# Kernel optimization log

Measured on AMD Instinct MI355X. Metric: run time of the kernel, lower is better.

Reference implementation:

```python
import jax, jax.numpy as jnp
import numpy as np

B, S, E, H, FFN, NQ = 4, 2048, 1024, 16, 4096, 8
DK = E // H
EPS = 1e-5


def setup_inputs() -> dict:
    key = jax.random.key(0)
    ks = jax.random.split(key, 8)
    x = jax.random.normal(ks[0], (B, S, E), dtype=jnp.float32)
    theta = jax.random.normal(ks[1], (NQ,), dtype=jnp.float32)  # RY angles
    w1 = jax.random.normal(ks[2], (FFN, NQ), dtype=jnp.float32) / np.sqrt(NQ)
    b1 = jnp.zeros((FFN,), dtype=jnp.float32)
    w2 = jax.random.normal(ks[3], (E, FFN), dtype=jnp.float32) / np.sqrt(FFN)
    b2 = jnp.zeros((E,), dtype=jnp.float32)
    gamma1 = jnp.ones((E,), dtype=jnp.float32)
    beta1 = jnp.zeros((E,), dtype=jnp.float32)
    gamma2 = jnp.ones((E,), dtype=jnp.float32)
    beta2 = jnp.zeros((E,), dtype=jnp.float32)
    return {"x": x, "theta": theta, "w1": w1, "b1": b1, "w2": w2, "b2": b2,
            "gamma1": gamma1, "beta1": beta1, "gamma2": gamma2, "beta2": beta2}


def _layernorm(h, g, b):
    mu = jnp.mean(h, axis=-1, keepdims=True)
    var = jnp.mean(jnp.square(h - mu), axis=-1, keepdims=True)
    return (h - mu) * jax.lax.rsqrt(var + EPS) * g + b


def _attention(x):
    # q = k = v = separate_heads(x); no projection weights in the original.
    q = x.reshape(B, S, H, DK).transpose(0, 2, 1, 3)  # [B,H,S,DK]
    scores = jnp.einsum("bhqd,bhkd->bhqk", q, q) / np.sqrt(DK)
    probs = jax.nn.softmax(scores, axis=-1)
    out = jnp.einsum("bhqk,bhkd->bhqd", probs, q)
    return out.transpose(0, 2, 1, 3).reshape(B, S, E)


def _ffn_quantum(h, theta, w1, b1, w2, b2):
    # Per-token circuit: RX(x_i) then RY(theta_i) on independent qubits,
    # measure PauliZ -> <Z_i> = cos(x_i) * cos(theta_i). Batched over all tokens.
    qout = jnp.cos(h[..., :NQ]) * jnp.cos(theta)  # [B,S,NQ]
    hid = jax.nn.relu(jnp.einsum("bsq,fq->bsf", qout, w1) + b1)
    return jnp.einsum("bsf,ef->bse", hid, w2) + b2


def reference(x, theta, w1, b1, w2, b2, gamma1, beta1, gamma2, beta2):
    attn_out = _attention(x)
    h = _layernorm(x + attn_out, gamma1, beta1)
    ffn_out = _ffn_quantum(h, theta, w1, b1, w2, b2)
    return _layernorm(h + ffn_out, gamma2, beta2)
```

## Files before the change

kernel.cpp:

```cpp
#include <hip/hip_runtime.h>


#define Bq 4
#define Sq 2048
#define Eq 1024
#define Hq 16
#define DKq 64
#define FFNq 4096
#define NQq 8
#define LOG2E 1.44269504f

typedef unsigned int u32;
typedef unsigned short u16;
typedef _Float16 f16;
typedef f16 f16x8 __attribute__((ext_vector_type(8)));
typedef __fp16 fp16x2 __attribute__((ext_vector_type(2)));
typedef float f32x4 __attribute__((ext_vector_type(4)));

#if __has_builtin(__builtin_amdgcn_exp2f)
#define EXP2F __builtin_amdgcn_exp2f
#else
#define EXP2F exp2f
#endif

#define MFMA(a, b, c) __builtin_amdgcn_mfma_f32_16x16x32_f16((a), (b), (c), 0, 0, 0)

#define GLL(g, l)                                                          \
  __builtin_amdgcn_global_load_lds(                                        \
      (const __attribute__((address_space(1))) u32*)(g),                   \
      (__attribute__((address_space(3))) u32*)(l), 16, 0, 0)

__device__ __forceinline__ u16 f2h(float x) {
  f16 t = (f16)x;
  return __builtin_bit_cast(u16, t);
}
__device__ __forceinline__ float h2f(u16 w) {
  return (float)__builtin_bit_cast(f16, w);
}
#if __has_builtin(__builtin_amdgcn_cvt_pkrtz)
__device__ __forceinline__ u32 pkrtz(float a, float b) {
  fp16x2 r = __builtin_amdgcn_cvt_pkrtz(a, b);
  return __builtin_bit_cast(u32, r);
}
#else
__device__ __forceinline__ u32 pkrtz(float a, float b) {
  return (u32)f2h(a) | ((u32)f2h(b) << 16);
}
#endif

union F8 { f16x8 v; u32 w[4]; u16 h[8]; f16 e[8]; };

__global__ void k_cvt(const float* __restrict__ src, uint4* __restrict__ dst, int n8) {
  int i = blockIdx.x * 256 + threadIdx.x;
  if (i >= n8) return;
  const float4* s = (const float4*)src + 2 * (long)i;
  float4 a = s[0], b = s[1];
  uint4 r;
  r.x = pkrtz(a.x, a.y);
  r.y = pkrtz(a.z, a.w);
  r.z = pkrtz(b.x, b.y);
  r.w = pkrtz(b.z, b.w);
  dst[i] = r;
}

__global__ void k_prep(const float* __restrict__ x, u16* __restrict__ xh,
                       u16* __restrict__ xt) {
  __shared__ u16 tile[64 * 72];
  const int tid = threadIdx.x;
  const int bx = blockIdx.x;
  const int sb = bx & 31, bh = bx >> 5;
  const int b = bh >> 4, h = bh & 15;
  const int s0 = sb * 64;
  const int r = tid >> 2, cq = tid & 3;
  const float* xp = x + ((long)(b * Sq + s0 + r)) * Eq + h * 64 + cq * 16;
  float4 f0 = ((const float4*)xp)[0], f1 = ((const float4*)xp)[1];
  float4 f2 = ((const float4*)xp)[2], f3 = ((const float4*)xp)[3];
  u32 w[8];
  w[0] = pkrtz(f0.x, f0.y); w[1] = pkrtz(f0.z, f0.w);
  w[2] = pkrtz(f1.x, f1.y); w[3] = pkrtz(f1.z, f1.w);
  w[4] = pkrtz(f2.x, f2.y); w[5] = pkrtz(f2.z, f2.w);
  w[6] = pkrtz(f3.x, f3.y); w[7] = pkrtz(f3.z, f3.w);
  uint4* xo = (uint4*)(xh + ((long)(b * Sq + s0 + r)) * Eq + h * 64 + cq * 16);
  xo[0] = make_uint4(w[0], w[1], w[2], w[3]);
  xo[1] = make_uint4(w[4], w[5], w[6], w[7]);
  uint4* tp = (uint4*)(tile + r * 72 + cq * 16);
  tp[0] = make_uint4(w[0], w[1], w[2], w[3]);
  tp[1] = make_uint4(w[4], w[5], w[6], w[7]);
  __syncthreads();
  const int d = tid >> 2, rq = tid & 3;
  u32 o[8];
#pragma unroll
  for (int i = 0; i < 8; ++i) {
    u32 lo = tile[(rq * 16 + 2 * i) * 72 + d];
    u32 hi = tile[(rq * 16 + 2 * i + 1) * 72 + d];
    o[i] = lo | (hi << 16);
  }
  uint4* to = (uint4*)(xt + ((long)(bh * 64 + d)) * Sq + s0 + rq * 16);
  to[0] = make_uint4(o[0], o[1], o[2], o[3]);
  to[1] = make_uint4(o[4], o[5], o[6], o[7]);
}

__global__ __launch_bounds__(512, 4) void k_attn(const u16* __restrict__ xh,
                                                 const u16* __restrict__ xt,
                                                 u16* __restrict__ attn) {
  __shared__ __align__(16) u16 lds[32768];
  u16* Pl = lds + 16384;

  const int tid = threadIdx.x;
  const int wave = tid >> 6, lane = tid & 63;
  const int n = lane & 15, quad = lane >> 4;

  const int bx = blockIdx.x;
  const int qb = bx >> 6, bh = bx & 63;
  const int b = bh >> 4, h = bh & 15;

  const u16* xh_bh = xh + (long)b * Sq * Eq + h * 64;
  const u16* xt_bh = xt + (long)bh * 64 * Sq;

  const float SC = 0.125f * LOG2E;
  F8 qf[2][2];
  float shift[2], lrow[2] = {0.f, 0.f};
#pragma unroll
  for (int nt = 0; nt < 2; ++nt) {
    const int q = qb * 256 + wave * 32 + nt * 16 + n;
    const u16* qp = xh_bh + (long)q * Eq + quad * 8;
    F8 a, c;
    a.v = *(const f16x8*)qp;
    c.v = *(const f16x8*)(qp + 32);
    float s2 = 0.f;
#pragma unroll
    for (int i = 0; i < 8; ++i) {
      float va = (float)a.e[i], vc = (float)c.e[i];
      s2 += va * va + vc * vc;
      qf[nt][0].e[i] = a.e[i] * (f16)SC;
      qf[nt][1].e[i] = c.e[i] * (f16)SC;
    }
    s2 += __shfl_xor(s2, 16);
    s2 += __shfl_xor(s2, 32);
    shift[nt] = SC * s2;
  }

  const int r8 = lane >> 3;
  const int cl = (lane & 7) ^ r8;
  const u16* gK = xh_bh + (long)(wave * 8 + r8) * Eq + cl * 8;
  const u16* gV = xt_bh + (long)(wave * 8 + r8) * Sq + cl * 8;
  const int lK = wave * 512;
  const int lV = 4096 + wave * 512;

  u16* cur = lds;
  u16* nxt = lds + 8192;

  GLL(gK, cur + lK);
  GLL(gV, cur + lV);
  gK += 64 * Eq;
  gV += 64;

  f32x4 O[2][4] = {};
  u16* Pw = Pl + wave * 2048;

  for (int kb = 0; kb < Sq / 64; ++kb) {
    __syncthreads();
    if (kb < Sq / 64 - 1) {
      GLL(gK, nxt + lK);
      GLL(gV, nxt + lV);
      gK += 64 * Eq;
      gV += 64;
    }
    u16* Kl = cur;
    u16* Vt = cur + 4096;

    f32x4 ST[2][4];
#pragma unroll
    for (int nt = 0; nt < 2; ++nt) {
      const float ms = -shift[nt];
#pragma unroll
      for (int mt = 0; mt < 4; ++mt) {
        ST[nt][mt][0] = ms; ST[nt][mt][1] = ms;
        ST[nt][mt][2] = ms; ST[nt][mt][3] = ms;
      }
    }
    __builtin_amdgcn_s_setprio(1);
#pragma unroll
    for (int mt = 0; mt < 4; ++mt) {
#pragma unroll
      for (int c = 0; c < 2; ++c) {
        f16x8 af = *(const f16x8*)(Kl + (mt * 16 + n) * 64 +
                                   (((c * 4 + quad) ^ (n & 7)) * 8));
#pragma unroll
        for (int nt = 0; nt < 2; ++nt)
          ST[nt][mt] = MFMA(af, qf[nt][c].v, ST[nt][mt]);
      }
    }
    __builtin_amdgcn_s_setprio(0);

#pragma unroll
    for (int nt = 0; nt < 2; ++nt) {
      float ls = 0.f;
#pragma unroll
      for (int mt = 0; mt < 4; ++mt) {
        float p0 = EXP2F(ST[nt][mt][0]);
        float p1 = EXP2F(ST[nt][mt][1]);
        float p2 = EXP2F(ST[nt][mt][2]);
        float p3 = EXP2F(ST[nt][mt][3]);
        ls += (p0 + p1) + (p2 + p3);
        const int ch = 2 * mt + (quad >> 1);
        *(uint2*)(Pw + nt * 1024 + n * 64 + ((ch ^ (n & 7)) * 8) + (quad & 1) * 4) =
            make_uint2(pkrtz(p0, p1), pkrtz(p2, p3));
      }
      lrow[nt] += ls;
    }

    __builtin_amdgcn_s_setprio(1);
#pragma unroll
    for (int c = 0; c < 2; ++c) {
      const int pc = ((c * 4 + quad) ^ (n & 7)) * 8;
      f16x8 pf[2];
#pragma unroll
      for (int nt = 0; nt < 2; ++nt)
        pf[nt] = *(const f16x8*)(Pw + nt * 1024 + n * 64 + pc);
#pragma unroll
      for (int dt = 0; dt < 4; ++dt) {
        f16x8 vf = *(const f16x8*)(Vt + (dt * 16 + n) * 64 + pc);
#pragma unroll
        for (int nt = 0; nt < 2; ++nt) O[nt][dt] = MFMA(vf, pf[nt], O[nt][dt]);
      }
    }
    __builtin_amdgcn_s_setprio(0);
    u16* t = cur; cur = nxt; nxt = t;
  }

#pragma unroll
  for (int nt = 0; nt < 2; ++nt) {
    float l = lrow[nt];
    l += __shfl_xor(l, 16);
    l += __shfl_xor(l, 32);
    const float inv = 1.0f / l;
    const int q = qb * 256 + wave * 32 + nt * 16 + n;
    u16* op = attn + (long)b * Sq * Eq + (long)q * Eq + h * 64;
#pragma unroll
    for (int dt = 0; dt < 4; ++dt) {
      u32 w0 = pkrtz(O[nt][dt][0] * inv, O[nt][dt][1] * inv);
      u32 w1 = pkrtz(O[nt][dt][2] * inv, O[nt][dt][3] * inv);
      *(uint2*)(op + dt * 16 + quad * 4) = make_uint2(w0, w1);
    }
  }
}

__global__ void k_ln1(const u16* __restrict__ xh, const u16* __restrict__ attn,
                      const float* __restrict__ g, const float* __restrict__ be,
                      const float* __restrict__ theta, u16* __restrict__ hout,
                      u16* __restrict__ qout) {
  const long t = blockIdx.x;
  const int tid = threadIdx.x;
  uint2 xw = ((const uint2*)(xh + t * Eq))[tid];
  uint2 aw = ((const uint2*)(attn + t * Eq))[tid];
  float v0 = h2f(xw.x & 0xffff) + h2f(aw.x & 0xffff);
  float v1 = h2f(xw.x >> 16) + h2f(aw.x >> 16);
  float v2 = h2f(xw.y & 0xffff) + h2f(aw.y & 0xffff);
  float v3 = h2f(xw.y >> 16) + h2f(aw.y >> 16);
  float s = (v0 + v1) + (v2 + v3);
  float s2 = v0 * v0 + v1 * v1 + v2 * v2 + v3 * v3;
#pragma unroll
  for (int o = 1; o < 64; o <<= 1) {
    s += __shfl_xor(s, o);
    s2 += __shfl_xor(s2, o);
  }
  __shared__ float red[8];
  const int wv = tid >> 6, ln = tid & 63;
  if (ln == 0) { red[wv] = s; red[4 + wv] = s2; }
  __syncthreads();
  s = red[0] + red[1] + red[2] + red[3];
  s2 = red[4] + red[5] + red[6] + red[7];
  const float mu = s * (1.f / Eq);
  const float var = s2 * (1.f / Eq) - mu * mu;
  const float rstd = rsqrtf(var + 1e-5f);
  float4 gv = ((const float4*)g)[tid];
  float4 bv = ((const float4*)be)[tid];
  float o0 = (v0 - mu) * rstd * gv.x + bv.x;
  float o1 = (v1 - mu) * rstd * gv.y + bv.y;
  float o2 = (v2 - mu) * rstd * gv.z + bv.z;
  float o3 = (v3 - mu) * rstd * gv.w + bv.w;
  ((uint2*)(hout + t * Eq))[tid] = make_uint2(pkrtz(o0, o1), pkrtz(o2, o3));
  if (tid < 2) {
    float hv[4] = {o0, o1, o2, o3};
    float q[4];
#pragma unroll
    for (int i = 0; i < 4; ++i) q[i] = cosf(hv[i]) * cosf(theta[tid * 4 + i]);
    *(uint2*)(qout + t * NQq + tid * 4) = make_uint2(pkrtz(q[0], q[1]), pkrtz(q[2], q[3]));
  }
}

__global__ void k_hid(const u16* __restrict__ qout, const float* __restrict__ w1,
                      const float* __restrict__ b1, u16* __restrict__ hid) {
  __shared__ float qs[256][8];
  const int tid = threadIdx.x;
  const int fb = blockIdx.x & 63, tb = blockIdx.x >> 6;
  const int f0 = fb * 64, t0 = tb * 256;
  {
    uint4 qw = *(const uint4*)(qout + (long)(t0 + tid) * NQq);
    qs[tid][0] = h2f(qw.x & 0xffff); qs[tid][1] = h2f(qw.x >> 16);
    qs[tid][2] = h2f(qw.y & 0xffff); qs[tid][3] = h2f(qw.y >> 16);
    qs[tid][4] = h2f(qw.z & 0xffff); qs[tid][5] = h2f(qw.z >> 16);
    qs[tid][6] = h2f(qw.w & 0xffff); qs[tid][7] = h2f(qw.w >> 16);
  }
  __syncthreads();
  const int wave = tid >> 6, lane = tid & 63;
  const int f = f0 + lane;
  const float4* wp = (const float4*)(w1 + (long)f * NQq);
  float4 wa = wp[0], wb = wp[1];
  const float bb = b1[f];
  const int trow = wave * 64;
  u16* op = hid + (long)(t0 + trow) * FFNq + f;
#pragma unroll 4
  for (int i = 0; i < 64; ++i) {
    const float* q = qs[trow + i];
    float acc = bb + q[0] * wa.x + q[1] * wa.y + q[2] * wa.z + q[3] * wa.w +
                q[4] * wb.x + q[5] * wb.y + q[6] * wb.z + q[7] * wb.w;
    acc = fmaxf(acc, 0.f);
    op[(long)i * FFNq] = f2h(acc);
  }
}

__global__ __launch_bounds__(256, 2) void k_gemm(const u16* __restrict__ Ah,
                                                 const u16* __restrict__ Bh,
                                                 u16* __restrict__ C) {
  __shared__ __align__(16) u16 lds[32768];
  const int tid = threadIdx.x;
  const int wave = tid >> 6, lane = tid & 63;
  const int n = lane & 15, quad = lane >> 4;
  const int wm = wave >> 1, wn = wave & 1;
  const int m0 = (blockIdx.x >> 3) * 128;
  const int n0 = (blockIdx.x & 7) * 128;
  const int r8 = lane >> 3;
  const int cl = (lane & 7) ^ r8;

  const u16* gA[4];
  const u16* gB[4];
  int lA[4], lB[4];
#pragma unroll
  for (int j = 0; j < 4; ++j) {
    const int row = wave * 32 + j * 8;
    gA[j] = Ah + (long)(m0 + row + r8) * FFNq + cl * 8;
    gB[j] = Bh + (long)(n0 + row + r8) * FFNq + cl * 8;
    lA[j] = row * 64;
    lB[j] = 8192 + row * 64;
  }

  u16* cur = lds;
  u16* nxt = lds + 16384;

#pragma unroll
  for (int j = 0; j < 4; ++j) {
    GLL(gA[j], cur + lA[j]);
    GLL(gB[j], cur + lB[j]);
    gA[j] += 64;
    gB[j] += 64;
  }

  f32x4 acc[4][4] = {};
  for (int it = 0; it < FFNq / 64; ++it) {
    __syncthreads();
    if (it < FFNq / 64 - 1) {
#pragma unroll
      for (int j = 0; j < 4; ++j) {
        GLL(gA[j], nxt + lA[j]);
        GLL(gB[j], nxt + lB[j]);
        gA[j] += 64;
        gB[j] += 64;
      }
    }
    u16* La = cur;
    u16* Lb = cur + 8192;
#pragma unroll
    for (int c = 0; c < 2; ++c) {
      f16x8 af[4], bf[4];
#pragma unroll
      for (int i = 0; i < 4; ++i) {
        const int ra = wm * 64 + i * 16 + n;
        const int rb = wn * 64 + i * 16 + n;
        af[i] = *(const f16x8*)(La + ra * 64 + (((c * 4 + quad) ^ (n & 7)) * 8));
        bf[i] = *(const f16x8*)(Lb + rb * 64 + (((c * 4 + quad) ^ (n & 7)) * 8));
      }
#pragma unroll
      for (int i = 0; i < 4; ++i)
#pragma unroll
        for (int j = 0; j < 4; ++j) acc[i][j] = MFMA(af[i], bf[j], acc[i][j]);
    }
    u16* t = cur; cur = nxt; nxt = t;
  }
#pragma unroll
  for (int i = 0; i < 4; ++i) {
    const int row = m0 + wm * 64 + i * 16 + quad * 4;
#pragma unroll
    for (int j = 0; j < 4; ++j) {
      u16* cp = C + (long)row * Eq + n0 + wn * 64 + j * 16 + n;
      cp[0] = f2h(acc[i][j][0]);
      cp[Eq] = f2h(acc[i][j][1]);
      cp[2 * Eq] = f2h(acc[i][j][2]);
      cp[3 * Eq] = f2h(acc[i][j][3]);
    }
  }
}

__global__ void k_ln2(const u16* __restrict__ hin, const u16* __restrict__ ffn,
                      const float* __restrict__ b2, const float* __restrict__ g,
                      const float* __restrict__ be, float* __restrict__ out) {
  const long t = blockIdx.x;
  const int tid = threadIdx.x;
  uint2 hw = ((const uint2*)(hin + t * Eq))[tid];
  uint2 fw = ((const uint2*)(ffn + t * Eq))[tid];
  float4 b2v = ((const float4*)b2)[tid];
  float v0 = h2f(hw.x & 0xffff) + h2f(fw.x & 0xffff) + b2v.x;
  float v1 = h2f(hw.x >> 16) + h2f(fw.x >> 16) + b2v.y;
  float v2 = h2f(hw.y & 0xffff) + h2f(fw.y & 0xffff) + b2v.z;
  float v3 = h2f(hw.y >> 16) + h2f(fw.y >> 16) + b2v.w;
  float s = (v0 + v1) + (v2 + v3);
  float s2 = v0 * v0 + v1 * v1 + v2 * v2 + v3 * v3;
#pragma unroll
  for (int o = 1; o < 64; o <<= 1) {
    s += __shfl_xor(s, o);
    s2 += __shfl_xor(s2, o);
  }
  __shared__ float red[8];
  const int wv = tid >> 6, ln = tid & 63;
  if (ln == 0) { red[wv] = s; red[4 + wv] = s2; }
  __syncthreads();
  s = red[0] + red[1] + red[2] + red[3];
  s2 = red[4] + red[5] + red[6] + red[7];
  const float mu = s * (1.f / Eq);
  const float var = s2 * (1.f / Eq) - mu * mu;
  const float rstd = rsqrtf(var + 1e-5f);
  float4 gv = ((const float4*)g)[tid];
  float4 bv = ((const float4*)be)[tid];
  float4 o;
  o.x = (v0 - mu) * rstd * gv.x + bv.x;
  o.y = (v1 - mu) * rstd * gv.y + bv.y;
  o.z = (v2 - mu) * rstd * gv.z + bv.z;
  o.w = (v3 - mu) * rstd * gv.w + bv.w;
  ((float4*)(out + t * Eq))[tid] = o;
}

extern "C" void kernel_launch(void* const* d_in, const int* in_sizes, int n_in,
                              void* d_out, int out_size, void* d_ws, size_t ws_size,
                              hipStream_t stream) {
  const float* x = (const float*)d_in[0];
  const float* theta = (const float*)d_in[1];
  const float* w1 = (const float*)d_in[2];
  const float* b1 = (const float*)d_in[3];
  const float* w2 = (const float*)d_in[4];
  const float* b2 = (const float*)d_in[5];
  const float* g1 = (const float*)d_in[6];
  const float* be1 = (const float*)d_in[7];
  const float* g2 = (const float*)d_in[8];
  const float* be2 = (const float*)d_in[9];
  float* out = (float*)d_out;

  char* ws = (char*)d_ws;
  u16* attn = (u16*)(ws);
  u16* h = (u16*)(ws + 16777216);
  u16* xh = (u16*)(ws + 33554432);
  u16* xt = (u16*)(ws + 50331648);
  u16* ffn = (u16*)(ws + 67108864);
  u16* hid = (u16*)(ws + 83886080);
  u16* w2h = (u16*)(ws + 150994944);
  u16* qout = (u16*)(ws + 159383552);

  k_prep<<<Bq * Hq * (Sq / 64), 256, 0, stream>>>(x, xh, xt);
  k_cvt<<<2048, 256, 0, stream>>>(w2, (uint4*)w2h, (Eq * FFNq) / 8);
  k_attn<<<Bq * Hq * (Sq / 256), 512, 0, stream>>>(xh, xt, attn);
  k_ln1<<<Bq * Sq, 256, 0, stream>>>(xh, attn, g1, be1, theta, h, qout);
  k_hid<<<(Bq * Sq / 256) * (FFNq / 64), 256, 0, stream>>>(qout, w1, b1, hid);
  k_gemm<<<(Bq * Sq / 128) * (Eq / 128), 256, 0, stream>>>(hid, w2h, ffn);
  k_ln2<<<Bq * Sq, 256, 0, stream>>>(h, ffn, b2, g2, be2, out);
}
```

Baseline: 311.1 us.

## Keep attention probabilities in registers using lane permutes instead of LDS round trip

```diff
diff --git a/kernel.cpp b/kernel.cpp
--- a/kernel.cpp
+++ b/kernel.cpp
@@ -16,6 +16,8 @@
 typedef f16 f16x8 __attribute__((ext_vector_type(8)));
 typedef __fp16 fp16x2 __attribute__((ext_vector_type(2)));
 typedef float f32x4 __attribute__((ext_vector_type(4)));
+typedef u32 u32x2 __attribute__((ext_vector_type(2)));
+typedef u32 u32x4 __attribute__((ext_vector_type(4)));
 
 #if __has_builtin(__builtin_amdgcn_exp2f)
 #define EXP2F __builtin_amdgcn_exp2f
@@ -47,6 +49,20 @@
   return (u32)f2h(a) | ((u32)f2h(b) << 16);
 }
 #endif
+
+__device__ __forceinline__ void swap32(u32 a, u32 b, u32& r0, u32& r1) {
+#if __has_builtin(__builtin_amdgcn_permlane32_swap)
+  u32x2 r = __builtin_amdgcn_permlane32_swap(a, b, false, false);
+  r0 = r[0];
+  r1 = r[1];
+#else
+  u32 ax = (u32)__shfl_xor((int)a, 32);
+  u32 bx = (u32)__shfl_xor((int)b, 32);
+  const bool lo = (threadIdx.x & 32) == 0;
+  r0 = lo ? a : bx;
+  r1 = lo ? ax : b;
+#endif
+}
 
 union F8 { f16x8 v; u32 w[4]; u16 h[8]; f16 e[8]; };
 
@@ -103,12 +119,12 @@
 __global__ __launch_bounds__(512, 4) void k_attn(const u16* __restrict__ xh,
                                                  const u16* __restrict__ xt,
                                                  u16* __restrict__ attn) {
-  __shared__ __align__(16) u16 lds[32768];
-  u16* Pl = lds + 16384;
+  __shared__ __align__(16) u16 lds[16384];
 
   const int tid = threadIdx.x;
   const int wave = tid >> 6, lane = tid & 63;
   const int n = lane & 15, quad = lane >> 4;
+  const bool quadEven = (quad & 1) == 0;
 
   const int bx = blockIdx.x;
   const int qb = bx >> 6, bh = bx & 63;
@@ -156,7 +172,6 @@
   gV += 64;
 
   f32x4 O[2][4] = {};
-  u16* Pw = Pl + wave * 2048;
 
   for (int kb = 0; kb < Sq / 64; ++kb) {
     __syncthreads();
@@ -193,8 +208,10 @@
     }
     __builtin_amdgcn_s_setprio(0);
 
+    f16x8 pfr[2][2];
 #pragma unroll
     for (int nt = 0; nt < 2; ++nt) {
+      u32 pk[8];
       float ls = 0.f;
 #pragma unroll
       for (int mt = 0; mt < 4; ++mt) {
@@ -203,26 +220,37 @@
         float p2 = EXP2F(ST[nt][mt][2]);
         float p3 = EXP2F(ST[nt][mt][3]);
         ls += (p0 + p1) + (p2 + p3);
-        const int ch = 2 * mt + (quad >> 1);
-        *(uint2*)(Pw + nt * 1024 + n * 64 + ((ch ^ (n & 7)) * 8) + (quad & 1) * 4) =
-            make_uint2(pkrtz(p0, p1), pkrtz(p2, p3));
+        pk[2 * mt] = pkrtz(p0, p1);
+        pk[2 * mt + 1] = pkrtz(p2, p3);
       }
       lrow[nt] += ls;
+#pragma unroll
+      for (int c = 0; c < 2; ++c) {
+        u32 r00, r10, r01, r11;
+        swap32(pk[4 * c + 0], pk[4 * c + 2], r00, r10);
+        swap32(pk[4 * c + 1], pk[4 * c + 3], r01, r11);
+        u32 U0 = quadEven ? r10 : r00;
+        u32 U1 = quadEven ? r11 : r01;
+        u32 Ux0 = (u32)__shfl_xor((int)U0, 16);
+        u32 Ux1 = (u32)__shfl_xor((int)U1, 16);
+        u32x4 wv;
+        wv[0] = quadEven ? r00 : Ux0;
+        wv[1] = quadEven ? r01 : Ux1;
+        wv[2] = quadEven ? Ux0 : r10;
+        wv[3] = quadEven ? Ux1 : r11;
+        pfr[nt][c] = __builtin_bit_cast(f16x8, wv);
+      }
     }
 
     __builtin_amdgcn_s_setprio(1);
 #pragma unroll
     for (int c = 0; c < 2; ++c) {
       const int pc = ((c * 4 + quad) ^ (n & 7)) * 8;
-      f16x8 pf[2];
-#pragma unroll
-      for (int nt = 0; nt < 2; ++nt)
-        pf[nt] = *(const f16x8*)(Pw + nt * 1024 + n * 64 + pc);
 #pragma unroll
       for (int dt = 0; dt < 4; ++dt) {
         f16x8 vf = *(const f16x8*)(Vt + (dt * 16 + n) * 64 + pc);
 #pragma unroll
-        for (int nt = 0; nt < 2; ++nt) O[nt][dt] = MFMA(vf, pf[nt], O[nt][dt]);
+        for (int nt = 0; nt < 2; ++nt) O[nt][dt] = MFMA(vf, pfr[nt][c], O[nt][dt]);
       }
     }
     __builtin_amdgcn_s_setprio(0);
```

After: 319.1 us. 2.6% more time.

## Fuse FFN hidden-layer computation into the second GEMM's A-tile production

Applied to the files above, without the earlier changes.

```diff
diff --git a/kernel.cpp b/kernel.cpp
--- a/kernel.cpp
+++ b/kernel.cpp
@@ -16,6 +16,7 @@
 typedef f16 f16x8 __attribute__((ext_vector_type(8)));
 typedef __fp16 fp16x2 __attribute__((ext_vector_type(2)));
 typedef float f32x4 __attribute__((ext_vector_type(4)));
+typedef u32 u32x4 __attribute__((ext_vector_type(4)));
 
 #if __has_builtin(__builtin_amdgcn_exp2f)
 #define EXP2F __builtin_amdgcn_exp2f
@@ -290,38 +291,9 @@
   }
 }
 
-__global__ void k_hid(const u16* __restrict__ qout, const float* __restrict__ w1,
-                      const float* __restrict__ b1, u16* __restrict__ hid) {
-  __shared__ float qs[256][8];
-  const int tid = threadIdx.x;
-  const int fb = blockIdx.x & 63, tb = blockIdx.x >> 6;
-  const int f0 = fb * 64, t0 = tb * 256;
-  {
-    uint4 qw = *(const uint4*)(qout + (long)(t0 + tid) * NQq);
-    qs[tid][0] = h2f(qw.x & 0xffff); qs[tid][1] = h2f(qw.x >> 16);
-    qs[tid][2] = h2f(qw.y & 0xffff); qs[tid][3] = h2f(qw.y >> 16);
-    qs[tid][4] = h2f(qw.z & 0xffff); qs[tid][5] = h2f(qw.z >> 16);
-    qs[tid][6] = h2f(qw.w & 0xffff); qs[tid][7] = h2f(qw.w >> 16);
-  }
-  __syncthreads();
-  const int wave = tid >> 6, lane = tid & 63;
-  const int f = f0 + lane;
-  const float4* wp = (const float4*)(w1 + (long)f * NQq);
-  float4 wa = wp[0], wb = wp[1];
-  const float bb = b1[f];
-  const int trow = wave * 64;
-  u16* op = hid + (long)(t0 + trow) * FFNq + f;
-#pragma unroll 4
-  for (int i = 0; i < 64; ++i) {
-    const float* q = qs[trow + i];
-    float acc = bb + q[0] * wa.x + q[1] * wa.y + q[2] * wa.z + q[3] * wa.w +
-                q[4] * wb.x + q[5] * wb.y + q[6] * wb.z + q[7] * wb.w;
-    acc = fmaxf(acc, 0.f);
-    op[(long)i * FFNq] = f2h(acc);
-  }
-}
-
-__global__ __launch_bounds__(256, 2) void k_gemm(const u16* __restrict__ Ah,
+__global__ __launch_bounds__(256, 2) void k_gemm(const u16* __restrict__ qout,
+                                                 const float* __restrict__ w1,
+                                                 const float* __restrict__ b1,
                                                  const u16* __restrict__ Bh,
                                                  u16* __restrict__ C) {
   __shared__ __align__(16) u16 lds[32768];
@@ -334,28 +306,62 @@
   const int r8 = lane >> 3;
   const int cl = (lane & 7) ^ r8;
 
-  const u16* gA[4];
   const u16* gB[4];
-  int lA[4], lB[4];
+  int lB[4];
 #pragma unroll
   for (int j = 0; j < 4; ++j) {
     const int row = wave * 32 + j * 8;
-    gA[j] = Ah + (long)(m0 + row + r8) * FFNq + cl * 8;
     gB[j] = Bh + (long)(n0 + row + r8) * FFNq + cl * 8;
-    lA[j] = row * 64;
     lB[j] = 8192 + row * 64;
   }
+
+  f16x8 qbf[8];
+#pragma unroll
+  for (int mt = 0; mt < 8; ++mt) {
+    u32x4 t = {0, 0, 0, 0};
+    if (quad == 0) {
+      const uint4 v = *(const uint4*)(qout + (long)(m0 + mt * 16 + n) * NQq);
+      t[0] = v.x; t[1] = v.y; t[2] = v.z; t[3] = v.w;
+    }
+    qbf[mt] = __builtin_bit_cast(f16x8, t);
+  }
+
+  auto computeA = [&](int it2, u16* buf) {
+    const int fbase = it2 * 64 + wave * 16;
+    u32x4 wfr = {0, 0, 0, 0};
+    if (quad == 0) {
+      const float4* wp = (const float4*)(w1 + (long)(fbase + n) * NQq);
+      const float4 a = wp[0], b = wp[1];
+      wfr[0] = pkrtz(a.x, a.y); wfr[1] = pkrtz(a.z, a.w);
+      wfr[2] = pkrtz(b.x, b.y); wfr[3] = pkrtz(b.z, b.w);
+    }
+    const f16x8 wf = __builtin_bit_cast(f16x8, wfr);
+    const float4 bias = *(const float4*)(b1 + fbase + quad * 4);
+    const int chunk = wave * 2 + (quad >> 1);
+    const int intra = (quad & 1) * 4;
+#pragma unroll
+    for (int mt = 0; mt < 8; ++mt) {
+      f32x4 zz = {0.f, 0.f, 0.f, 0.f};
+      f32x4 g = MFMA(wf, qbf[mt], zz);
+      const float h0 = fmaxf(g[0] + bias.x, 0.f);
+      const float h1 = fmaxf(g[1] + bias.y, 0.f);
+      const float h2 = fmaxf(g[2] + bias.z, 0.f);
+      const float h3 = fmaxf(g[3] + bias.w, 0.f);
+      const int m = mt * 16 + n;
+      *(uint2*)(buf + m * 64 + ((chunk ^ (m & 7)) * 8) + intra) =
+          make_uint2(pkrtz(h0, h1), pkrtz(h2, h3));
+    }
+  };
 
   u16* cur = lds;
   u16* nxt = lds + 16384;
 
 #pragma unroll
   for (int j = 0; j < 4; ++j) {
-    GLL(gA[j], cur + lA[j]);
     GLL(gB[j], cur + lB[j]);
-    gA[j] += 64;
     gB[j] += 64;
   }
+  computeA(0, cur);
 
   f32x4 acc[4][4] = {};
   for (int it = 0; it < FFNq / 64; ++it) {
@@ -363,11 +369,10 @@
     if (it < FFNq / 64 - 1) {
 #pragma unroll
       for (int j = 0; j < 4; ++j) {
-        GLL(gA[j], nxt + lA[j]);
         GLL(gB[j], nxt + lB[j]);
-        gA[j] += 64;
         gB[j] += 64;
       }
+      computeA(it + 1, nxt);
     }
     u16* La = cur;
     u16* Lb = cur + 8192;
@@ -461,7 +466,6 @@
   u16* xh = (u16*)(ws + 33554432);
   u16* xt = (u16*)(ws + 50331648);
   u16* ffn = (u16*)(ws + 67108864);
-  u16* hid = (u16*)(ws + 83886080);
   u16* w2h = (u16*)(ws + 150994944);
   u16* qout = (u16*)(ws + 159383552);
 
@@ -469,7 +473,6 @@
   k_cvt<<<2048, 256, 0, stream>>>(w2, (uint4*)w2h, (Eq * FFNq) / 8);
   k_attn<<<Bq * Hq * (Sq / 256), 512, 0, stream>>>(xh, xt, attn);
   k_ln1<<<Bq * Sq, 256, 0, stream>>>(xh, attn, g1, be1, theta, h, qout);
-  k_hid<<<(Bq * Sq / 256) * (FFNq / 64), 256, 0, stream>>>(qout, w1, b1, hid);
-  k_gemm<<<(Bq * Sq / 128) * (Eq / 128), 256, 0, stream>>>(hid, w2h, ffn);
+  k_gemm<<<(Bq * Sq / 128) * (Eq / 128), 256, 0, stream>>>(qout, w1, b1, w2h, ffn);
   k_ln2<<<Bq * Sq, 256, 0, stream>>>(h, ffn, b2, g2, be2, out);
 }
```

After: 319.4 us. 2.6% more time.

## Merge w2 conversion into prep kernel and shrink FFN GEMM tile to 64x128

Applied to the files above, without the earlier changes.

```diff
diff --git a/kernel.cpp b/kernel.cpp
--- a/kernel.cpp
+++ b/kernel.cpp
@@ -50,24 +50,27 @@
 
 union F8 { f16x8 v; u32 w[4]; u16 h[8]; f16 e[8]; };
 
-__global__ void k_cvt(const float* __restrict__ src, uint4* __restrict__ dst, int n8) {
-  int i = blockIdx.x * 256 + threadIdx.x;
-  if (i >= n8) return;
-  const float4* s = (const float4*)src + 2 * (long)i;
-  float4 a = s[0], b = s[1];
-  uint4 r;
-  r.x = pkrtz(a.x, a.y);
-  r.y = pkrtz(a.z, a.w);
-  r.z = pkrtz(b.x, b.y);
-  r.w = pkrtz(b.z, b.w);
-  dst[i] = r;
-}
-
 __global__ void k_prep(const float* __restrict__ x, u16* __restrict__ xh,
-                       u16* __restrict__ xt) {
+                       u16* __restrict__ xt, const float* __restrict__ w2src,
+                       uint4* __restrict__ w2dst) {
   __shared__ u16 tile[64 * 72];
   const int tid = threadIdx.x;
   const int bx = blockIdx.x;
+  if (bx >= 2048) {
+    const int i = (bx - 2048) * 256 + tid;
+    const int n8 = (Eq * FFNq) / 8;
+    if (i < n8) {
+      const float4* s = (const float4*)w2src + 2 * (long)i;
+      float4 a = s[0], b = s[1];
+      uint4 r;
+      r.x = pkrtz(a.x, a.y);
+      r.y = pkrtz(a.z, a.w);
+      r.z = pkrtz(b.x, b.y);
+      r.w = pkrtz(b.z, b.w);
+      w2dst[i] = r;
+    }
+    return;
+  }
   const int sb = bx & 31, bh = bx >> 5;
   const int b = bh >> 4, h = bh & 15;
   const int s0 = sb * 64;
@@ -321,79 +324,65 @@
   }
 }
 
-__global__ __launch_bounds__(256, 2) void k_gemm(const u16* __restrict__ Ah,
+__global__ __launch_bounds__(256, 4) void k_gemm(const u16* __restrict__ Ah,
                                                  const u16* __restrict__ Bh,
                                                  u16* __restrict__ C) {
-  __shared__ __align__(16) u16 lds[32768];
+  __shared__ __align__(16) u16 lds[12288];
   const int tid = threadIdx.x;
   const int wave = tid >> 6, lane = tid & 63;
   const int n = lane & 15, quad = lane >> 4;
-  const int wm = wave >> 1, wn = wave & 1;
-  const int m0 = (blockIdx.x >> 3) * 128;
+  const int m0 = (blockIdx.x >> 3) * 64;
   const int n0 = (blockIdx.x & 7) * 128;
   const int r8 = lane >> 3;
   const int cl = (lane & 7) ^ r8;
 
-  const u16* gA[4];
+  const u16* gA0 = Ah + (long)(m0 + wave * 16 + r8) * FFNq + cl * 8;
+  const u16* gA1 = gA0 + 8 * FFNq;
+  const int lA0 = (wave * 16) * 64, lA1 = (wave * 16 + 8) * 64;
   const u16* gB[4];
-  int lA[4], lB[4];
-#pragma unroll
-  for (int j = 0; j < 4; ++j) {
-    const int row = wave * 32 + j * 8;
-    gA[j] = Ah + (long)(m0 + row + r8) * FFNq + cl * 8;
-    gB[j] = Bh + (long)(n0 + row + r8) * FFNq + cl * 8;
-    lA[j] = row * 64;
-    lB[j] = 8192 + row * 64;
-  }
-
-  u16* cur = lds;
-  u16* nxt = lds + 16384;
-
-#pragma unroll
-  for (int j = 0; j < 4; ++j) {
-    GLL(gA[j], cur + lA[j]);
-    GLL(gB[j], cur + lB[j]);
-    gA[j] += 64;
-    gB[j] += 64;
-  }
-
-  f32x4 acc[4][4] = {};
+  int lB[4];
+#pragma unroll
+  for (int u = 0; u < 4; ++u) {
+    const int row = wave * 32 + u * 8;
+    gB[u] = Bh + (long)(n0 + row + r8) * FFNq + cl * 8;
+    lB[u] = 4096 + row * 64;
+  }
+
+  f32x4 acc[4][2] = {};
   for (int it = 0; it < FFNq / 64; ++it) {
+    GLL(gA0, lds + lA0);
+    GLL(gA1, lds + lA1);
+#pragma unroll
+    for (int u = 0; u < 4; ++u) GLL(gB[u], lds + lB[u]);
+    gA0 += 64; gA1 += 64;
+#pragma unroll
+    for (int u = 0; u < 4; ++u) gB[u] += 64;
     __syncthreads();
-    if (it < FFNq / 64 - 1) {
-#pragma unroll
-      for (int j = 0; j < 4; ++j) {
-        GLL(gA[j], nxt + lA[j]);
-        GLL(gB[j], nxt + lB[j]);
-        gA[j] += 64;
-        gB[j] += 64;
-      }
-    }
-    u16* La = cur;
-    u16* Lb = cur + 8192;
+    u16* La = lds;
+    u16* Lb = lds + 4096;
 #pragma unroll
     for (int c = 0; c < 2; ++c) {
-      f16x8 af[4], bf[4];
-#pragma unroll
-      for (int i = 0; i < 4; ++i) {
-        const int ra = wm * 64 + i * 16 + n;
-        const int rb = wn * 64 + i * 16 + n;
-        af[i] = *(const f16x8*)(La + ra * 64 + (((c * 4 + quad) ^ (n & 7)) * 8));
-        bf[i] = *(const f16x8*)(Lb + rb * 64 + (((c * 4 + quad) ^ (n & 7)) * 8));
-      }
+      const int sw = ((c * 4 + quad) ^ (n & 7)) * 8;
+      f16x8 af[4], bf[2];
 #pragma unroll
       for (int i = 0; i < 4; ++i)
-#pragma unroll
-        for (int j = 0; j < 4; ++j) acc[i][j] = MFMA(af[i], bf[j], acc[i][j]);
-    }
-    u16* t = cur; cur = nxt; nxt = t;
+        af[i] = *(const f16x8*)(La + (i * 16 + n) * 64 + sw);
+#pragma unroll
+      for (int j = 0; j < 2; ++j)
+        bf[j] = *(const f16x8*)(Lb + (wave * 32 + j * 16 + n) * 64 + sw);
+#pragma unroll
+      for (int i = 0; i < 4; ++i)
+#pragma unroll
+        for (int j = 0; j < 2; ++j) acc[i][j] = MFMA(af[i], bf[j], acc[i][j]);
+    }
+    __syncthreads();
   }
 #pragma unroll
   for (int i = 0; i < 4; ++i) {
-    const int row = m0 + wm * 64 + i * 16 + quad * 4;
-#pragma unroll
-    for (int j = 0; j < 4; ++j) {
-      u16* cp = C + (long)row * Eq + n0 + wn * 64 + j * 16 + n;
+    const int row = m0 + i * 16 + quad * 4;
+#pragma unroll
+    for (int j = 0; j < 2; ++j) {
+      u16* cp = C + (long)row * Eq + n0 + wave * 32 + j * 16 + n;
       cp[0] = f2h(acc[i][j][0]);
       cp[Eq] = f2h(acc[i][j][1]);
       cp[2 * Eq] = f2h(acc[i][j][2]);
@@ -465,11 +454,10 @@
   u16* w2h = (u16*)(ws + 150994944);
   u16* qout = (u16*)(ws + 159383552);
 
-  k_prep<<<Bq * Hq * (Sq / 64), 256, 0, stream>>>(x, xh, xt);
-  k_cvt<<<2048, 256, 0, stream>>>(w2, (uint4*)w2h, (Eq * FFNq) / 8);
+  k_prep<<<2 * Bq * Hq * (Sq / 64), 256, 0, stream>>>(x, xh, xt, w2, (uint4*)w2h);
   k_attn<<<Bq * Hq * (Sq / 256), 512, 0, stream>>>(xh, xt, attn);
   k_ln1<<<Bq * Sq, 256, 0, stream>>>(xh, attn, g1, be1, theta, h, qout);
   k_hid<<<(Bq * Sq / 256) * (FFNq / 64), 256, 0, stream>>>(qout, w1, b1, hid);
-  k_gemm<<<(Bq * Sq / 128) * (Eq / 128), 256, 0, stream>>>(hid, w2h, ffn);
+  k_gemm<<<(Bq * Sq / 64) * (Eq / 128), 256, 0, stream>>>(hid, w2h, ffn);
   k_ln2<<<Bq * Sq, 256, 0, stream>>>(h, ffn, b2, g2, be2, out);
 }
```

Result: slower. 324.6 us (+4.3%).
